# Performance work log

Hardware: AMD Instinct MI355X
Metric: run time of the kernel (lower is better)

Reference implementation:

```python
import jax, jax.numpy as jnp
import numpy as np

B = 4096
IN = 1024
H = 1024
S = 64   # num_memory_slots
Q = 16   # num_qubits_per_slot
OUT = 1024


def setup_inputs() -> dict:
    key = jax.random.key(0)
    ks = jax.random.split(key, 14)
    sd = lambda fan_in: 1.0 / np.sqrt(fan_in)
    return {
        "x_t": jax.random.normal(ks[0], (B, IN), jnp.float32),
        "h_prev": jax.random.normal(ks[1], (B, H), jnp.float32),
        # input_layer: Linear(IN+H, H)
        "W_in": jax.random.normal(ks[2], (IN + H, H), jnp.float32) * sd(IN + H),
        "b_in": jnp.zeros((H,), jnp.float32),
        # query_generator: Linear(H, H)
        "W_q": jax.random.normal(ks[3], (H, H), jnp.float32) * sd(H),
        "b_q": jnp.zeros((H,), jnp.float32),
        # memory_slot_selector: Linear(H, S)
        "W_sel": jax.random.normal(ks[4], (H, S), jnp.float32) * sd(H),
        "b_sel": jnp.zeros((S,), jnp.float32),
        # per-slot quantum memory params (surrogate classical simulation):
        # encode hidden -> qubit rotation angles, expectation <Z>=cos(angle), decode back
        "Wm_enc": jax.random.normal(ks[5], (S, H, Q), jnp.float32) * sd(H),
        "theta": jax.random.normal(ks[6], (S, Q), jnp.float32) * 0.1,
        "Wm_dec": jax.random.normal(ks[7], (S, Q, H), jnp.float32) * sd(Q),
        "b_m": jnp.zeros((H,), jnp.float32),
        # output_gate_and_transform: Linear(2H, H+OUT)
        "W_og": jax.random.normal(ks[8], (2 * H, H + OUT), jnp.float32) * sd(2 * H),
        "b_og": jnp.zeros((H + OUT,), jnp.float32),
    }


def reference(x_t, h_prev, W_in, b_in, W_q, b_q, W_sel, b_sel,
              Wm_enc, theta, Wm_dec, b_m, W_og, b_og):
    # combined input -> intermediate hidden
    combined = jnp.concatenate([x_t, h_prev], axis=1)           # (B, IN+H)
    h_int = jnp.tanh(combined @ W_in + b_in)                    # (B, H)
    # attention query -> slot logits -> top-1 slot per sample
    query = h_int @ W_q + b_q                                   # (B, H)
    logits = query @ W_sel + b_sel                              # (B, S)
    attn = jax.nn.softmax(logits, axis=1)
    idx = jnp.argmax(attn, axis=1)                              # (B,) int
    # batched gather-compute (replaces Python loop over batch)
    Wi = Wm_enc[idx]                                            # (B, H, Q)
    th = theta[idx]                                             # (B, Q)
    Wo = Wm_dec[idx]                                            # (B, Q, H)
    angles = jnp.einsum('bh,bhq->bq', h_int, Wi) + th           # (B, Q)
    expz = jnp.cos(angles)                                      # qubit <Z> expectations
    m_t = jnp.tanh(jnp.einsum('bq,bqh->bh', expz, Wo) + b_m)    # (B, H)
    # gated output + next hidden
    combined_out = jnp.concatenate([h_int, m_t], axis=1)        # (B, 2H)
    goh = combined_out @ W_og + b_og                            # (B, H+OUT)
    h_next = jnp.tanh(goh[:, :H])
    y_t = goh[:, H:]
    return (y_t, h_next)
```

## Files before the change

### kernel.cpp

```cpp
#include <hip/hip_runtime.h>
#include <math.h>


typedef __attribute__((ext_vector_type(4))) float floatx4;
typedef __attribute__((ext_vector_type(8))) _Float16 half8;
typedef __attribute__((ext_vector_type(4))) _Float16 half4;

#define OUT_H_OFF 4194304
#define TAU 4e-3f
#define FIX_CAP 512

#define AS1 __attribute__((address_space(1)))
#define AS3 __attribute__((address_space(3)))
#define GLL(gptr, lptr) __builtin_amdgcn_global_load_lds((const AS1 void*)(gptr), (AS3 void*)(lptr), 16, 0, 0)

__device__ __forceinline__ _Float16 f2h(float f) { return (_Float16)f; }

__global__ __launch_bounds__(256) void k_transpose(const float* __restrict__ W,
                                                   _Float16* __restrict__ BT) {
  __shared__ float tile[64][65];
  const int k0 = blockIdx.x * 64, n0 = blockIdx.y * 64;
  const int t = threadIdx.x, c = t & 63, rr = t >> 6;
#pragma unroll
  for (int i = 0; i < 16; ++i) {
    int r = i * 4 + rr;
    tile[r][c] = W[(size_t)(k0 + r) * 2048 + n0 + c];
  }
  __syncthreads();
#pragma unroll
  for (int i = 0; i < 16; ++i) {
    int r = i * 4 + rr;
    BT[(size_t)(n0 + r) * 2048 + k0 + c] = f2h(tile[c][r]);
  }
}

__global__ __launch_bounds__(256) void k_convA(const float* __restrict__ x_t, const float* __restrict__ h_prev,
                                               _Float16* __restrict__ A1) {
  const int stride = gridDim.x * blockDim.x;
  for (int c = blockIdx.x * blockDim.x + threadIdx.x; c < 2097152; c += stride) {
    int m = c >> 9, kc = (c & 511) << 2;
    const float* src = (kc < 1024) ? (x_t + (size_t)m * 1024 + kc)
                                   : (h_prev + (size_t)m * 1024 + (kc - 1024));
    floatx4 v = *reinterpret_cast<const floatx4*>(src);
    half4 h = {f2h(v[0]), f2h(v[1]), f2h(v[2]), f2h(v[3])};
    *reinterpret_cast<half4*>(&A1[(size_t)m * 2048 + kc]) = h;
  }
}

__global__ __launch_bounds__(256) void k_convB(const float* __restrict__ W_in,
                                               _Float16* __restrict__ BTin) {
  __shared__ float tile[64][65];
  const int k0 = blockIdx.x * 64, n0 = blockIdx.y * 64;
  const int t = threadIdx.x, c = t & 63, rr = t >> 6;
#pragma unroll
  for (int i = 0; i < 16; ++i) {
    int r = i * 4 + rr;
    tile[r][c] = W_in[(size_t)(k0 + r) * 1024 + n0 + c];
  }
  __syncthreads();
#pragma unroll
  for (int i = 0; i < 16; ++i) {
    int r = i * 4 + rr;
    BTin[(size_t)(n0 + r) * 2048 + k0 + c] = f2h(tile[c][r]);
  }
}

__global__ __launch_bounds__(256) void k_gemm1h(const _Float16* __restrict__ A1,
                                                const _Float16* __restrict__ BTin,
                                                const float* __restrict__ b_in,
                                                _Float16* __restrict__ A2) {
  __shared__ __align__(16) _Float16 As[4 * 4096];
  __shared__ __align__(16) _Float16 Bs[4 * 2048];
  const int t = threadIdx.x;
  const int lane = t & 63, w = t >> 6;
  const int wm = w >> 1, wn = w & 1;
  const int m0 = blockIdx.x * 128, n0 = blockIdx.y * 64;
  const int lr = lane & 15, lk = lane >> 4;
  floatx4 acc[4][2];
  floatx4 zero = {0.f, 0.f, 0.f, 0.f};
#pragma unroll
  for (int mi = 0; mi < 4; ++mi)
#pragma unroll
    for (int ni = 0; ni < 2; ++ni) acc[mi][ni] = zero;

  auto stage = [&](int p, int kt) {
    const int k0 = kt * 32;
#pragma unroll
    for (int j = 0; j < 2; ++j) {
      int cc = j * 256 + t;
      int row = cc >> 2, sl = cc & 3;
      int sg = sl ^ ((row >> 1) & 3);
      size_t ga = (size_t)(m0 + row) * 2048 + k0 + sg * 8;
      GLL(A1 + ga, &As[p * 4096 + cc * 8]);
    }
    {
      int cc = t;
      int row = cc >> 2, sl = cc & 3;
      int sg = sl ^ ((row >> 1) & 3);
      size_t gb = (size_t)(n0 + row) * 2048 + k0 + sg * 8;
      GLL(BTin + gb, &Bs[p * 2048 + cc * 8]);
    }
  };
  auto compute = [&](int p) {
    half8 af[4], bf[2];
#pragma unroll
    for (int mi = 0; mi < 4; ++mi) {
      int row = wm * 64 + mi * 16 + lr;
      int sl = lk ^ ((row >> 1) & 3);
      af[mi] = *reinterpret_cast<const half8*>(&As[p * 4096 + row * 32 + sl * 8]);
    }
#pragma unroll
    for (int ni = 0; ni < 2; ++ni) {
      int row = wn * 32 + ni * 16 + lr;
      int sl = lk ^ ((row >> 1) & 3);
      bf[ni] = *reinterpret_cast<const half8*>(&Bs[p * 2048 + row * 32 + sl * 8]);
    }
#pragma unroll
    for (int mi = 0; mi < 4; ++mi)
#pragma unroll
      for (int ni = 0; ni < 2; ++ni)
        acc[mi][ni] = __builtin_amdgcn_mfma_f32_16x16x32_f16(af[mi], bf[ni], acc[mi][ni], 0, 0, 0);
  };

  stage(0, 0);
  stage(1, 1);
  stage(2, 2);
  for (int kt = 0; kt < 64; ++kt) {
    __builtin_amdgcn_sched_barrier(0);
    if (kt < 62) {
      asm volatile("s_waitcnt vmcnt(6)" ::: "memory");
    } else if (kt == 62) {
      asm volatile("s_waitcnt vmcnt(3)" ::: "memory");
    } else {
      asm volatile("s_waitcnt vmcnt(0)" ::: "memory");
    }
    __builtin_amdgcn_s_barrier();
    __builtin_amdgcn_sched_barrier(0);
    if (kt + 3 < 64) stage((kt + 3) & 3, kt + 3);
    compute(kt & 3);
  }

#pragma unroll
  for (int mi = 0; mi < 4; ++mi) {
#pragma unroll
    for (int ni = 0; ni < 2; ++ni) {
      int gn = n0 + wn * 32 + ni * 16 + lr;
      float bias = b_in[gn];
      int gmb = m0 + wm * 64 + mi * 16 + lk * 4;
#pragma unroll
      for (int j = 0; j < 4; ++j) {
        int gm = gmb + j;
        A2[(size_t)gm * 2048 + gn] = f2h(tanhf(acc[mi][ni][j] + bias));
      }
    }
  }
}

__global__ __launch_bounds__(256) void k_gemm1(const float* __restrict__ x_t, const float* __restrict__ h_prev,
                                               const float* __restrict__ W_in, const float* __restrict__ b_in,
                                               _Float16* __restrict__ A2) {
  __shared__ float As[16 * 128];
  __shared__ float Bs[16 * 64];
  const int t = threadIdx.x;
  const int m0 = blockIdx.x * 128, n0 = blockIdx.y * 64;
  const int ty = t >> 4, tx = t & 15;
  float acc[8][4];
#pragma unroll
  for (int i = 0; i < 8; ++i)
#pragma unroll
    for (int j = 0; j < 4; ++j) acc[i][j] = 0.f;
  for (int kt = 0; kt < 128; ++kt) {
    const int k0 = kt * 16;
    __syncthreads();
#pragma unroll
    for (int u = 0; u < 2; ++u) {
      int cc = t + u * 256;
      int row = cc >> 2, col4 = (cc & 3) << 2;
      int gk = k0 + col4;
      const float* src = (gk < 1024) ? (x_t + (size_t)(m0 + row) * 1024 + gk)
                                     : (h_prev + (size_t)(m0 + row) * 1024 + (gk - 1024));
      floatx4 v = *reinterpret_cast<const floatx4*>(src);
      As[(col4 + 0) * 128 + row] = v[0];
      As[(col4 + 1) * 128 + row] = v[1];
      As[(col4 + 2) * 128 + row] = v[2];
      As[(col4 + 3) * 128 + row] = v[3];
    }
    {
      int kr = t >> 4, c4 = (t & 15) << 2;
      *reinterpret_cast<floatx4*>(&Bs[kr * 64 + c4]) =
          *reinterpret_cast<const floatx4*>(&W_in[(size_t)(k0 + kr) * 1024 + n0 + c4]);
    }
    __syncthreads();
#pragma unroll
    for (int kk = 0; kk < 16; ++kk) {
      floatx4 a0 = *reinterpret_cast<const floatx4*>(&As[kk * 128 + ty * 8]);
      floatx4 a1 = *reinterpret_cast<const floatx4*>(&As[kk * 128 + ty * 8 + 4]);
      floatx4 b = *reinterpret_cast<const floatx4*>(&Bs[kk * 64 + tx * 4]);
#pragma unroll
      for (int j = 0; j < 4; ++j) {
        acc[0][j] += a0[0] * b[j]; acc[1][j] += a0[1] * b[j];
        acc[2][j] += a0[2] * b[j]; acc[3][j] += a0[3] * b[j];
        acc[4][j] += a1[0] * b[j]; acc[5][j] += a1[1] * b[j];
        acc[6][j] += a1[2] * b[j]; acc[7][j] += a1[3] * b[j];
      }
    }
  }
  const int nbase = n0 + tx * 4;
  floatx4 bias = *reinterpret_cast<const floatx4*>(&b_in[nbase]);
#pragma unroll
  for (int i = 0; i < 8; ++i) {
    int gm = m0 + ty * 8 + i;
    half4 pk;
#pragma unroll
    for (int j = 0; j < 4; ++j) pk[j] = f2h(tanhf(acc[i][j] + bias[j]));
    *reinterpret_cast<half4*>(&A2[(size_t)gm * 2048 + nbase]) = pk;
  }
}

__global__ __launch_bounds__(256) void k_wqs(const float* __restrict__ W_q, const float* __restrict__ b_q,
                                             const float* __restrict__ W_sel, const float* __restrict__ b_sel,
                                             float* __restrict__ Wqs) {
  const int t = threadIdx.x;
  const int w = t >> 6, lane = t & 63;
  const int h = blockIdx.x * 4 + w;
  if (h > 1024) return;
  const float* src = (h < 1024) ? (W_q + (size_t)h * 1024) : b_q;
  float acc = 0.f;
  for (int j = 0; j < 1024; j += 4) {
    floatx4 v = *reinterpret_cast<const floatx4*>(&src[j]);
    acc += v[0] * W_sel[(j + 0) * 64 + lane];
    acc += v[1] * W_sel[(j + 1) * 64 + lane];
    acc += v[2] * W_sel[(j + 2) * 64 + lane];
    acc += v[3] * W_sel[(j + 3) * 64 + lane];
  }
  if (h == 1024) acc += b_sel[lane];
  Wqs[(size_t)h * 64 + lane] = acc;
}

__global__ __launch_bounds__(256) void k_argmax(const _Float16* __restrict__ A2, const float* __restrict__ Wqs,
                                                int* __restrict__ idx, int* __restrict__ counter,
                                                int* __restrict__ list, float tau) {
  __shared__ float Ahs[64 * 17];
  __shared__ float Wt[64 * 64];
  const int t = threadIdx.x;
  const int r0 = blockIdx.x * 16;
  const int w = t >> 6, lane = t & 63;
  float acc[4] = {0.f, 0.f, 0.f, 0.f};

  for (int kt = 0; kt < 16; ++kt) {
    const int k0 = kt * 64;
    __syncthreads();
    if (t < 128) {
      int r = t >> 3, k8 = (t & 7) * 8;
      half8 v = *reinterpret_cast<const half8*>(&A2[(size_t)(r0 + r) * 2048 + k0 + k8]);
#pragma unroll
      for (int j = 0; j < 8; ++j) Ahs[(k8 + j) * 17 + r] = (float)v[j];
    }
#pragma unroll
    for (int u = 0; u < 4; ++u) {
      int cc = t + u * 256;
      int kr = cc >> 4, c4 = (cc & 15) << 2;
      *reinterpret_cast<floatx4*>(&Wt[kr * 64 + c4]) =
          *reinterpret_cast<const floatx4*>(&Wqs[(size_t)(k0 + kr) * 64 + c4]);
    }
    __syncthreads();
#pragma unroll
    for (int k = 0; k < 64; ++k) {
      float wv = Wt[k * 64 + lane];
      const float* ar = &Ahs[k * 17 + w * 4];
      acc[0] += ar[0] * wv;
      acc[1] += ar[1] * wv;
      acc[2] += ar[2] * wv;
      acc[3] += ar[3] * wv;
    }
  }
  const float bqs = Wqs[1024 * 64 + lane];
#pragma unroll
  for (int i = 0; i < 4; ++i) {
    float v1 = acc[i] + bqs;
    int i1 = lane;
    float v2 = -__builtin_inff();
#pragma unroll
    for (int off = 32; off >= 1; off >>= 1) {
      float ov1 = __shfl_xor(v1, off);
      int oi1 = __shfl_xor(i1, off);
      float ov2 = __shfl_xor(v2, off);
      if (ov1 > v1 || (ov1 == v1 && oi1 < i1)) {
        v2 = fmaxf(v1, ov2); v1 = ov1; i1 = oi1;
      } else {
        v2 = fmaxf(v2, ov1);
      }
    }
    if (lane == 0) {
      int row = r0 + w * 4 + i;
      idx[row] = i1;
      if (v1 - v2 < tau) {
        int pos = atomicAdd(counter, 1);
        if (pos < FIX_CAP) list[pos] = row;
      }
    }
  }
}

__global__ __launch_bounds__(256) void k_fixA3(const float* __restrict__ x_t, const float* __restrict__ h_prev,
                                               const float* __restrict__ W_in, const int* __restrict__ counter,
                                               const int* __restrict__ list, float* __restrict__ scratch) {
  __shared__ float Ws[256 * 64];
  __shared__ float xr[8][260];
  const int t = threadIdx.x;
  const int cnt = min(counter[0], FIX_CAP);
  const int nbatch = (cnt + 7) >> 3;
  const int col = t & 63;
  const int rp = t >> 6;
  const int gcol = blockIdx.x * 64 + col;
  for (int mb = blockIdx.y; mb < nbatch; mb += gridDim.y) {
    const int rbase = mb * 8;
    float a0[4] = {0.f, 0.f, 0.f, 0.f};
    float a1[4] = {0.f, 0.f, 0.f, 0.f};
    for (int kc = 0; kc < 8; ++kc) {
      __syncthreads();
      {
        int r = t >> 5, kl = (t & 31) * 8;
        int e = rbase + r;
        int row = list[e < cnt ? e : 0];
        int kg = kc * 256 + kl;
        const float* src = (kg < 1024) ? (x_t + (size_t)row * 1024 + kg)
                                       : (h_prev + (size_t)row * 1024 + (kg - 1024));
        floatx4 v0 = *reinterpret_cast<const floatx4*>(src);
        floatx4 v1 = *reinterpret_cast<const floatx4*>(src + 4);
        *reinterpret_cast<floatx4*>(&xr[r][kl]) = v0;
        *reinterpret_cast<floatx4*>(&xr[r][kl + 4]) = v1;
      }
      {
        const float* Wb = W_in + (size_t)(kc * 256) * 1024 + blockIdx.x * 64;
#pragma unroll
        for (int i = 0; i < 16; ++i) {
          int f = t + 256 * i;
          int k = f >> 4, c4 = (f & 15) << 2;
          floatx4 v = *reinterpret_cast<const floatx4*>(Wb + (size_t)k * 1024 + c4);
          *reinterpret_cast<floatx4*>(&Ws[k * 64 + c4]) = v;
        }
      }
      __syncthreads();
      const floatx4* x0v = reinterpret_cast<const floatx4*>(xr[rp * 2]);
      const floatx4* x1v = reinterpret_cast<const floatx4*>(xr[rp * 2 + 1]);
      for (int k4 = 0; k4 < 64; ++k4) {
        floatx4 xv0 = x0v[k4];
        floatx4 xv1 = x1v[k4];
        int kb = k4 * 4;
        float w0 = Ws[(kb + 0) * 64 + col];
        float w1 = Ws[(kb + 1) * 64 + col];
        float w2 = Ws[(kb + 2) * 64 + col];
        float w3 = Ws[(kb + 3) * 64 + col];
        a0[0] += xv0[0] * w0; a1[0] += xv1[0] * w0;
        a0[1] += xv0[1] * w1; a1[1] += xv1[1] * w1;
        a0[2] += xv0[2] * w2; a1[2] += xv1[2] * w2;
        a0[3] += xv0[3] * w3; a1[3] += xv1[3] * w3;
      }
    }
    float z0 = (a0[0] + a0[1]) + (a0[2] + a0[3]);
    float z1 = (a1[0] + a1[1]) + (a1[2] + a1[3]);
    int e0 = rbase + rp * 2, e1 = e0 + 1;
    if (e0 < cnt) scratch[(size_t)e0 * 1024 + gcol] = z0;
    if (e1 < cnt) scratch[(size_t)e1 * 1024 + gcol] = z1;
    __syncthreads();
  }
}

__global__ __launch_bounds__(256) void k_fixB(const float* __restrict__ scratch, const float* __restrict__ b_in,
                                              const float* __restrict__ Wqs, const int* __restrict__ counter,
                                              const int* __restrict__ list, int* __restrict__ idx) {
  __shared__ float hrow[1024];
  __shared__ float partial[4 * 64];
  __shared__ float lg[64];
  const int t = threadIdx.x;
  const int cnt = min(counter[0], FIX_CAP);
  const int e = blockIdx.x;
  if (e >= cnt) return;
  const int r = list[e];
  const int n4 = t * 4;
  floatx4 b4 = *reinterpret_cast<const floatx4*>(&b_in[n4]);
  floatx4 z4 = *reinterpret_cast<const floatx4*>(&scratch[(size_t)e * 1024 + n4]);
  hrow[n4 + 0] = tanhf(z4[0] + b4[0]);
  hrow[n4 + 1] = tanhf(z4[1] + b4[1]);
  hrow[n4 + 2] = tanhf(z4[2] + b4[2]);
  hrow[n4 + 3] = tanhf(z4[3] + b4[3]);
  __syncthreads();
  const int s = t & 63, part = t >> 6;
  const int hb0 = part * 256;
  const float* Wp = Wqs + (size_t)hb0 * 64 + s;
  float p0 = 0.f, p1 = 0.f, p2 = 0.f, p3 = 0.f, p4 = 0.f, p5 = 0.f, p6 = 0.f, p7 = 0.f;
  for (int h8 = 0; h8 < 256; h8 += 8) {
    float w0 = Wp[(size_t)(h8 + 0) * 64];
    float w1 = Wp[(size_t)(h8 + 1) * 64];
    float w2 = Wp[(size_t)(h8 + 2) * 64];
    float w3 = Wp[(size_t)(h8 + 3) * 64];
    float w4 = Wp[(size_t)(h8 + 4) * 64];
    float w5 = Wp[(size_t)(h8 + 5) * 64];
    float w6 = Wp[(size_t)(h8 + 6) * 64];
    float w7 = Wp[(size_t)(h8 + 7) * 64];
    const int hb = hb0 + h8;
    p0 += hrow[hb + 0] * w0;
    p1 += hrow[hb + 1] * w1;
    p2 += hrow[hb + 2] * w2;
    p3 += hrow[hb + 3] * w3;
    p4 += hrow[hb + 4] * w4;
    p5 += hrow[hb + 5] * w5;
    p6 += hrow[hb + 6] * w6;
    p7 += hrow[hb + 7] * w7;
  }
  partial[part * 64 + s] = ((p0 + p1) + (p2 + p3)) + ((p4 + p5) + (p6 + p7));
  __syncthreads();
  if (t < 64) lg[t] = partial[t] + partial[64 + t] + partial[128 + t] + partial[192 + t] + Wqs[1024 * 64 + t];
  __syncthreads();
  if (t == 0) {
    float bv = lg[0]; int bi = 0;
    for (int ss = 1; ss < 64; ++ss) {
      if (lg[ss] > bv) { bv = lg[ss]; bi = ss; }
    }
    idx[r] = bi;
  }
}

__global__ __launch_bounds__(256) void k_mix(const _Float16* __restrict__ A2h, const int* __restrict__ idx,
                                             const float* __restrict__ Wm_enc, const float* __restrict__ theta,
                                             const float* __restrict__ Wm_dec, const float* __restrict__ b_m,
                                             _Float16* __restrict__ A2) {
  __shared__ float hrow[1024];
  __shared__ float partial[256];
  __shared__ float expz[16];
  const int b = blockIdx.x, t = threadIdx.x;
  const int s = idx[b];
  {
    half4 v = *reinterpret_cast<const half4*>(&A2h[(size_t)b * 2048 + t * 4]);
    hrow[t * 4 + 0] = (float)v[0];
    hrow[t * 4 + 1] = (float)v[1];
    hrow[t * 4 + 2] = (float)v[2];
    hrow[t * 4 + 3] = (float)v[3];
  }
  __syncthreads();
  const int q = t & 15, g = t >> 4;
  const float* We = Wm_enc + (size_t)s * 16384;
  float p = 0.f;
#pragma unroll 8
  for (int j = 0; j < 64; ++j) {
    int h = g + j * 16;
    p += hrow[h] * We[h * 16 + q];
  }
  partial[t] = p;
  __syncthreads();
  if (t < 16) {
    float a = 0.f;
#pragma unroll
    for (int g2 = 0; g2 < 16; ++g2) a += partial[g2 * 16 + t];
    a += theta[s * 16 + t];
    expz[t] = cosf(a);
  }
  __syncthreads();
  const float* Wd = Wm_dec + (size_t)s * 16384;
  float e[16];
#pragma unroll
  for (int qq = 0; qq < 16; ++qq) e[qq] = expz[qq];
#pragma unroll
  for (int r = 0; r < 4; ++r) {
    int h = r * 256 + t;
    float v = b_m[h];
#pragma unroll
    for (int qq = 0; qq < 16; ++qq) v += e[qq] * Wd[qq * 1024 + h];
    A2[(size_t)b * 2048 + 1024 + h] = f2h(tanhf(v));
  }
}

__global__ __launch_bounds__(256) void k_gemm4h(const _Float16* __restrict__ A2,
                                                const _Float16* __restrict__ BT,
                                                const float* __restrict__ b_og, float* __restrict__ out) {
  __shared__ __align__(16) _Float16 As[4 * 4096];
  __shared__ __align__(16) _Float16 Bs[4 * 4096];
  const int t = threadIdx.x;
  const int lane = t & 63, w = t >> 6;
  const int wm = w >> 1, wn = w & 1;
  const int m0 = blockIdx.x * 128, n0 = blockIdx.y * 128;
  const int lr = lane & 15, lk = lane >> 4;
  floatx4 acc[4][4];
  floatx4 zero = {0.f, 0.f, 0.f, 0.f};
#pragma unroll
  for (int mi = 0; mi < 4; ++mi)
#pragma unroll
    for (int ni = 0; ni < 4; ++ni) acc[mi][ni] = zero;

  auto stage = [&](int p, int kt) {
    const int k0 = kt * 32;
#pragma unroll
    for (int j = 0; j < 2; ++j) {
      int cc = j * 256 + t;
      int row = cc >> 2, sl = cc & 3;
      int sg = sl ^ ((row >> 1) & 3);
      size_t ga = (size_t)(m0 + row) * 2048 + k0 + sg * 8;
      size_t gb = (size_t)(n0 + row) * 2048 + k0 + sg * 8;
      GLL(A2 + ga, &As[p * 4096 + cc * 8]);
      GLL(BT + gb, &Bs[p * 4096 + cc * 8]);
    }
  };
  auto compute = [&](int p) {
    half8 af[4], bf[4];
#pragma unroll
    for (int mi = 0; mi < 4; ++mi) {
      int row = wm * 64 + mi * 16 + lr;
      int sl = lk ^ ((row >> 1) & 3);
      af[mi] = *reinterpret_cast<const half8*>(&As[p * 4096 + row * 32 + sl * 8]);
    }
#pragma unroll
    for (int ni = 0; ni < 4; ++ni) {
      int row = wn * 64 + ni * 16 + lr;
      int sl = lk ^ ((row >> 1) & 3);
      bf[ni] = *reinterpret_cast<const half8*>(&Bs[p * 4096 + row * 32 + sl * 8]);
    }
#pragma unroll
    for (int mi = 0; mi < 4; ++mi)
#pragma unroll
      for (int ni = 0; ni < 4; ++ni)
        acc[mi][ni] = __builtin_amdgcn_mfma_f32_16x16x32_f16(af[mi], bf[ni], acc[mi][ni], 0, 0, 0);
  };

  stage(0, 0);
  stage(1, 1);
  stage(2, 2);
  for (int kt = 0; kt < 64; ++kt) {
    __builtin_amdgcn_sched_barrier(0);
    if (kt < 62) {
      asm volatile("s_waitcnt vmcnt(8)" ::: "memory");
    } else if (kt == 62) {
      asm volatile("s_waitcnt vmcnt(4)" ::: "memory");
    } else {
      asm volatile("s_waitcnt vmcnt(0)" ::: "memory");
    }
    __builtin_amdgcn_s_barrier();
    __builtin_amdgcn_sched_barrier(0);
    if (kt + 3 < 64) stage((kt + 3) & 3, kt + 3);
    compute(kt & 3);
  }

#pragma unroll
  for (int mi = 0; mi < 4; ++mi) {
#pragma unroll
    for (int ni = 0; ni < 4; ++ni) {
      int gn = n0 + wn * 64 + ni * 16 + lr;
      float bias = b_og[gn];
      int gmb = m0 + wm * 64 + mi * 16 + lk * 4;
#pragma unroll
      for (int j = 0; j < 4; ++j) {
        int gm = gmb + j;
        float v = acc[mi][ni][j] + bias;
        if (gn < 1024) {
          out[OUT_H_OFF + (size_t)gm * 1024 + gn] = tanhf(v);
        } else {
          out[(size_t)gm * 1024 + (gn - 1024)] = v;
        }
      }
    }
  }
}

extern "C" void kernel_launch(void* const* d_in, const int* in_sizes, int n_in,
                              void* d_out, int out_size, void* d_ws, size_t ws_size,
                              hipStream_t stream) {
  (void)in_sizes; (void)n_in; (void)out_size;
  const float* x_t    = (const float*)d_in[0];
  const float* h_prev = (const float*)d_in[1];
  const float* W_in   = (const float*)d_in[2];
  const float* b_in   = (const float*)d_in[3];
  const float* W_q    = (const float*)d_in[4];
  const float* b_q    = (const float*)d_in[5];
  const float* W_sel  = (const float*)d_in[6];
  const float* b_sel  = (const float*)d_in[7];
  const float* Wm_enc = (const float*)d_in[8];
  const float* theta  = (const float*)d_in[9];
  const float* Wm_dec = (const float*)d_in[10];
  const float* b_m    = (const float*)d_in[11];
  const float* W_og   = (const float*)d_in[12];
  const float* b_og   = (const float*)d_in[13];
  float* out = (float*)d_out;

  char* ws = (char*)d_ws;
  _Float16* A2          = (_Float16*)(ws + ((size_t)16 << 20));
  _Float16* BT          = (_Float16*)(ws + ((size_t)32 << 20));
  float* Wqs            = (float*)(ws + ((size_t)40 << 20));
  int* idx              = (int*)(ws + ((size_t)41 << 20));
  int* counter          = (int*)(ws + ((size_t)41 << 20) + 16384);
  int* list             = (int*)(ws + ((size_t)41 << 20) + 16384 + 64);
  _Float16* A1          = (_Float16*)(ws + ((size_t)42 << 20));
  _Float16* BTin        = (_Float16*)(ws + ((size_t)58 << 20));
  float* fix_scratch    = (float*)(ws + ((size_t)62 << 20));

  const bool use_mfma = ws_size >= ((size_t)82 << 20);

  hipLaunchKernelGGL(k_transpose, dim3(32, 32), dim3(256), 0, stream, W_og, BT);
  hipLaunchKernelGGL(k_wqs, dim3(257), dim3(256), 0, stream, W_q, b_q, W_sel, b_sel, Wqs);
  hipMemsetAsync(counter, 0, 4, stream);

  if (use_mfma) {
    hipLaunchKernelGGL(k_convA, dim3(2048), dim3(256), 0, stream, x_t, h_prev, A1);
    hipLaunchKernelGGL(k_convB, dim3(32, 16), dim3(256), 0, stream, W_in, BTin);
    hipLaunchKernelGGL(k_gemm1h, dim3(32, 16), dim3(256), 0, stream,
                       A1, BTin, b_in, A2);
    hipLaunchKernelGGL(k_argmax, dim3(256), dim3(256), 0, stream, A2, Wqs, idx, counter, list, TAU);
    hipLaunchKernelGGL(k_fixA3, dim3(16, 32), dim3(256), 0, stream,
                       x_t, h_prev, W_in, counter, list, fix_scratch);
    hipLaunchKernelGGL(k_fixB, dim3(FIX_CAP), dim3(256), 0, stream,
                       fix_scratch, b_in, Wqs, counter, list, idx);
  } else {
    hipLaunchKernelGGL(k_gemm1, dim3(32, 16), dim3(256), 0, stream, x_t, h_prev, W_in, b_in, A2);
    hipLaunchKernelGGL(k_argmax, dim3(256), dim3(256), 0, stream, A2, Wqs, idx, counter, list, 0.0f);
  }

  hipLaunchKernelGGL(k_mix, dim3(4096), dim3(256), 0, stream, A2, idx, Wm_enc, theta, Wm_dec, b_m, A2);
  hipLaunchKernelGGL(k_gemm4h, dim3(32, 16), dim3(256), 0, stream, A2, BT, b_og, out);
}
```

Measured before the change: 263.5 us.

## Load A fragments directly to registers and shrink B LDS pipeline to double buffer

In both fp16 MFMA GEMMs, the A operand is no longer staged through LDS. Each lane now loads its half8 fragments straight from global memory into registers, and only B keeps LDS staging. B drops from a 4-stage to a 2-stage buffer with __syncthreads ping-pong, replacing the hand-tuned vmcnt waits and the 3-deep prefetch. This cuts LDS traffic and footprint, which may raise occupancy. The cost is shallower prefetch, less coalesced per-lane global loads for A, more vector registers, and reliance on the compiler to wait on the loads.

```diff
diff --git a/kernel.cpp b/kernel.cpp
--- a/kernel.cpp
+++ b/kernel.cpp
@@ -69,8 +69,7 @@
                                                 const _Float16* __restrict__ BTin,
                                                 const float* __restrict__ b_in,
                                                 _Float16* __restrict__ A2) {
-  __shared__ __align__(16) _Float16 As[4 * 4096];
-  __shared__ __align__(16) _Float16 Bs[4 * 2048];
+  __shared__ __align__(16) _Float16 Bs[2 * 2048];
   const int t = threadIdx.x;
   const int lane = t & 63, w = t >> 6;
   const int wm = w >> 1, wn = w & 1;
@@ -83,32 +82,27 @@
 #pragma unroll
     for (int ni = 0; ni < 2; ++ni) acc[mi][ni] = zero;
 
-  auto stage = [&](int p, int kt) {
+  const _Float16* Abase[4];
+#pragma unroll
+  for (int mi = 0; mi < 4; ++mi)
+    Abase[mi] = A1 + (size_t)(m0 + wm * 64 + mi * 16 + lr) * 2048 + lk * 8;
+
+  auto stageB = [&](int p, int kt) {
     const int k0 = kt * 32;
-#pragma unroll
-    for (int j = 0; j < 2; ++j) {
-      int cc = j * 256 + t;
-      int row = cc >> 2, sl = cc & 3;
-      int sg = sl ^ ((row >> 1) & 3);
-      size_t ga = (size_t)(m0 + row) * 2048 + k0 + sg * 8;
-      GLL(A1 + ga, &As[p * 4096 + cc * 8]);
-    }
-    {
-      int cc = t;
-      int row = cc >> 2, sl = cc & 3;
-      int sg = sl ^ ((row >> 1) & 3);
-      size_t gb = (size_t)(n0 + row) * 2048 + k0 + sg * 8;
-      GLL(BTin + gb, &Bs[p * 2048 + cc * 8]);
-    }
+    int cc = t;
+    int row = cc >> 2, sl = cc & 3;
+    int sg = sl ^ ((row >> 1) & 3);
+    size_t gb = (size_t)(n0 + row) * 2048 + k0 + sg * 8;
+    GLL(BTin + gb, &Bs[p * 2048 + cc * 8]);
   };
-  auto compute = [&](int p) {
-    half8 af[4], bf[2];
-#pragma unroll
-    for (int mi = 0; mi < 4; ++mi) {
-      int row = wm * 64 + mi * 16 + lr;
-      int sl = lk ^ ((row >> 1) & 3);
-      af[mi] = *reinterpret_cast<const half8*>(&As[p * 4096 + row * 32 + sl * 8]);
-    }
+  auto loadA = [&](half8* af, int kt) {
+    const int k0 = kt * 32;
+#pragma unroll
+    for (int mi = 0; mi < 4; ++mi)
+      af[mi] = *reinterpret_cast<const half8*>(Abase[mi] + k0);
+  };
+  auto compute = [&](int p, const half8* af) {
+    half8 bf[2];
 #pragma unroll
     for (int ni = 0; ni < 2; ++ni) {
       int row = wn * 32 + ni * 16 + lr;
@@ -122,22 +116,21 @@
         acc[mi][ni] = __builtin_amdgcn_mfma_f32_16x16x32_f16(af[mi], bf[ni], acc[mi][ni], 0, 0, 0);
   };
 
-  stage(0, 0);
-  stage(1, 1);
-  stage(2, 2);
-  for (int kt = 0; kt < 64; ++kt) {
-    __builtin_amdgcn_sched_barrier(0);
-    if (kt < 62) {
-      asm volatile("s_waitcnt vmcnt(6)" ::: "memory");
-    } else if (kt == 62) {
-      asm volatile("s_waitcnt vmcnt(3)" ::: "memory");
-    } else {
-      asm volatile("s_waitcnt vmcnt(0)" ::: "memory");
-    }
-    __builtin_amdgcn_s_barrier();
-    __builtin_amdgcn_sched_barrier(0);
-    if (kt + 3 < 64) stage((kt + 3) & 3, kt + 3);
-    compute(kt & 3);
+  half8 afA[4], afB[4];
+  stageB(0, 0);
+  loadA(afA, 0);
+  __syncthreads();
+  for (int kt2 = 0; kt2 < 64; kt2 += 2) {
+    stageB(1, kt2 + 1);
+    loadA(afB, kt2 + 1);
+    compute(0, afA);
+    __syncthreads();
+    if (kt2 + 2 < 64) {
+      stageB(0, kt2 + 2);
+      loadA(afA, kt2 + 2);
+    }
+    compute(1, afB);
+    __syncthreads();
   }
 
 #pragma unroll
@@ -474,8 +467,7 @@
 __global__ __launch_bounds__(256) void k_gemm4h(const _Float16* __restrict__ A2,
                                                 const _Float16* __restrict__ BT,
                                                 const float* __restrict__ b_og, float* __restrict__ out) {
-  __shared__ __align__(16) _Float16 As[4 * 4096];
-  __shared__ __align__(16) _Float16 Bs[4 * 4096];
+  __shared__ __align__(16) _Float16 Bs[2 * 4096];
   const int t = threadIdx.x;
   const int lane = t & 63, w = t >> 6;
   const int wm = w >> 1, wn = w & 1;
@@ -488,27 +480,30 @@
 #pragma unroll
     for (int ni = 0; ni < 4; ++ni) acc[mi][ni] = zero;
 
-  auto stage = [&](int p, int kt) {
+  const _Float16* Abase[4];
+#pragma unroll
+  for (int mi = 0; mi < 4; ++mi)
+    Abase[mi] = A2 + (size_t)(m0 + wm * 64 + mi * 16 + lr) * 2048 + lk * 8;
+
+  auto stageB = [&](int p, int kt) {
     const int k0 = kt * 32;
 #pragma unroll
     for (int j = 0; j < 2; ++j) {
       int cc = j * 256 + t;
       int row = cc >> 2, sl = cc & 3;
       int sg = sl ^ ((row >> 1) & 3);
-      size_t ga = (size_t)(m0 + row) * 2048 + k0 + sg * 8;
       size_t gb = (size_t)(n0 + row) * 2048 + k0 + sg * 8;
-      GLL(A2 + ga, &As[p * 4096 + cc * 8]);
       GLL(BT + gb, &Bs[p * 4096 + cc * 8]);
     }
   };
-  auto compute = [&](int p) {
-    half8 af[4], bf[4];
-#pragma unroll
-    for (int mi = 0; mi < 4; ++mi) {
-      int row = wm * 64 + mi * 16 + lr;
-      int sl = lk ^ ((row >> 1) & 3);
-      af[mi] = *reinterpret_cast<const half8*>(&As[p * 4096 + row * 32 + sl * 8]);
-    }
+  auto loadA = [&](half8* af, int kt) {
+    const int k0 = kt * 32;
+#pragma unroll
+    for (int mi = 0; mi < 4; ++mi)
+      af[mi] = *reinterpret_cast<const half8*>(Abase[mi] + k0);
+  };
+  auto compute = [&](int p, const half8* af) {
+    half8 bf[4];
 #pragma unroll
     for (int ni = 0; ni < 4; ++ni) {
       int row = wn * 64 + ni * 16 + lr;
@@ -522,22 +517,21 @@
         acc[mi][ni] = __builtin_amdgcn_mfma_f32_16x16x32_f16(af[mi], bf[ni], acc[mi][ni], 0, 0, 0);
   };
 
-  stage(0, 0);
-  stage(1, 1);
-  stage(2, 2);
-  for (int kt = 0; kt < 64; ++kt) {
-    __builtin_amdgcn_sched_barrier(0);
-    if (kt < 62) {
-      asm volatile("s_waitcnt vmcnt(8)" ::: "memory");
-    } else if (kt == 62) {
-      asm volatile("s_waitcnt vmcnt(4)" ::: "memory");
-    } else {
-      asm volatile("s_waitcnt vmcnt(0)" ::: "memory");
-    }
-    __builtin_amdgcn_s_barrier();
-    __builtin_amdgcn_sched_barrier(0);
-    if (kt + 3 < 64) stage((kt + 3) & 3, kt + 3);
-    compute(kt & 3);
+  half8 afA[4], afB[4];
+  stageB(0, 0);
+  loadA(afA, 0);
+  __syncthreads();
+  for (int kt2 = 0; kt2 < 64; kt2 += 2) {
+    stageB(1, kt2 + 1);
+    loadA(afB, kt2 + 1);
+    compute(0, afA);
+    __syncthreads();
+    if (kt2 + 2 < 64) {
+      stageB(0, kt2 + 2);
+      loadA(afA, kt2 + 2);
+    }
+    compute(1, afB);
+    __syncthreads();
   }
 
 #pragma unroll
```

New measurement: 315.6 us. 1.2x slower.
